# Kernel tuning notes

Measured on AMD Instinct MI355X. Metric: run time of the kernel, lower is better.

Reference implementation:

```python
import jax, jax.numpy as jnp
import numpy as np
import math

TIN = 4          # patch_size
NF = 128         # num_features
DM = 256         # d_model
NH = 8           # n_heads
HD = DM // NH    # head_dim = 32
FF = 1024        # ff_dim
NL = 4           # num_layers
MAXD = 64        # max_rel_dist -> L = 129


def _ln(x, g, b, eps):
    mu = jnp.mean(x, axis=-1, keepdims=True)
    var = jnp.mean(jnp.square(x - mu), axis=-1, keepdims=True)
    return (x - mu) * jax.lax.rsqrt(var + eps) * g + b


def setup_inputs() -> dict:
    key = jax.random.key(0)
    ks = jax.random.split(key, 24)
    s = 0.02
    d = {
        'x': jax.random.normal(ks[0], (2000, 16, NF), jnp.float32),
        'ln1_g': jnp.ones((TIN * NF,), jnp.float32),
        'ln1_b': jnp.zeros((TIN * NF,), jnp.float32),
        'proj_w': jax.random.normal(ks[1], (TIN * NF, DM), jnp.float32) * s,
        'proj_b': jnp.zeros((DM,), jnp.float32),
        'ln2_g': jnp.ones((DM,), jnp.float32),
        'ln2_b': jnp.zeros((DM,), jnp.float32),
        'rel_bias': jax.random.normal(ks[2], (NH, 2 * MAXD + 1), jnp.float32) * s,
        'ln_attn_g': jnp.ones((NL, DM), jnp.float32),
        'ln_attn_b': jnp.zeros((NL, DM), jnp.float32),
        'qkv_w': jax.random.normal(ks[3], (NL, DM, 3 * DM), jnp.float32) * s,
        'qkv_b': jnp.zeros((NL, 3 * DM), jnp.float32),
        'out_w': jax.random.normal(ks[4], (NL, DM, DM), jnp.float32) * s,
        'out_b': jnp.zeros((NL, DM), jnp.float32),
        'ln_ff_g': jnp.ones((NL, DM), jnp.float32),
        'ln_ff_b': jnp.zeros((NL, DM), jnp.float32),
        'ff1_w': jax.random.normal(ks[5], (NL, DM, FF), jnp.float32) * s,
        'ff1_b': jnp.zeros((NL, FF), jnp.float32),
        'ff2_w': jax.random.normal(ks[6], (NL, FF, DM), jnp.float32) * s,
        'ff2_b': jnp.zeros((NL, DM), jnp.float32),
        'fln_g': jnp.ones((DM,), jnp.float32),
        'fln_b': jnp.zeros((DM,), jnp.float32),
        'op_w': jax.random.normal(ks[7], (DM, NF), jnp.float32) * s,
        'op_b': jnp.zeros((NF,), jnp.float32),
    }
    return d


def reference(x, ln1_g, ln1_b, proj_w, proj_b, ln2_g, ln2_b, rel_bias,
              ln_attn_g, ln_attn_b, qkv_w, qkv_b, out_w, out_b,
              ln_ff_g, ln_ff_b, ff1_w, ff1_b, ff2_w, ff2_b,
              fln_g, fln_b, op_w, op_b):
    # ---- PatchEmbedding ----
    h = jnp.swapaxes(x, 0, 1)                 # [B, T, F]
    B, T, F = h.shape
    n_patch = T // TIN                        # 500 (== chunk_size, single chunk path)
    h = h[:, :n_patch * TIN, :].reshape(B, n_patch, TIN * F)
    h = _ln(h, ln1_g, ln1_b, 1e-6)
    h = h @ proj_w + proj_b
    h = _ln(h, ln2_g, ln2_b, 1e-6)            # [B, S, DM]
    S = n_patch

    # ---- relative position bias [H, S, S] ----
    pos = jnp.arange(S)
    rel = pos[None, :] - pos[:, None]
    idx = jnp.clip(rel, -MAXD, MAXD) + MAXD
    bias = rel_bias[:, idx]                   # [H, S, S]

    # ---- causal mask ----
    causal = jnp.triu(jnp.full((S, S), -jnp.inf, jnp.float32), k=1)
    scale = 1.0 / math.sqrt(HD)

    for l in range(NL):
        # attention block
        a = _ln(h, ln_attn_g[l], ln_attn_b[l], 1e-5)
        qkv = a @ qkv_w[l] + qkv_b[l]         # [B, S, 3*DM]
        q, k, v = jnp.split(qkv, 3, axis=-1)
        q = q.reshape(B, S, NH, HD)
        k = k.reshape(B, S, NH, HD)
        v = v.reshape(B, S, NH, HD)
        scores = jnp.einsum('bihd,bjhd->bhij', q, k) * scale
        scores = scores + bias[None] + causal
        attn = jax.nn.softmax(scores, axis=-1)
        o = jnp.einsum('bhij,bjhd->bihd', attn, v).reshape(B, S, DM)
        h = h + (o @ out_w[l] + out_b[l])
        # ffn block
        f = _ln(h, ln_ff_g[l], ln_ff_b[l], 1e-5)
        f = jax.nn.gelu(f @ ff1_w[l] + ff1_b[l], approximate=False)
        h = h + (f @ ff2_w[l] + ff2_b[l])

    h = _ln(h, fln_g, fln_b, 1e-5)
    h = h @ op_w + op_b                       # [B, S, NF]
    return jnp.swapaxes(h, 0, 1)              # [S, B, NF]
```

## Files before the change

### kernel.cpp

```cpp
#include <hip/hip_runtime.h>

#define TS 500
#define NB 16
#define NROW 8000
#define DMODEL 256
#define NHEAD 8
#define HDIM 32
#define FFD 1024

typedef __bf16 bf16x8 __attribute__((ext_vector_type(8)));
typedef __bf16 bf16x4 __attribute__((ext_vector_type(4)));
typedef float  f32x4  __attribute__((ext_vector_type(4)));
typedef float  f32x2  __attribute__((ext_vector_type(2)));

__device__ __forceinline__ float wred_sum(float v) {
    #pragma unroll
    for (int off = 32; off; off >>= 1) v += __shfl_xor(v, off, 64);
    return v;
}

__device__ __forceinline__ void pa_store(__bf16* __restrict__ PA, int KS,
                                         int grow, int col, float y) {
    int mt = grow >> 4, rl = grow & 15;
    size_t idx = ((size_t)(mt * KS + (col >> 5)) * 64 + ((col >> 3) & 3) * 16 + rl) * 8 + (col & 7);
    PA[idx] = (__bf16)y;
}

__global__ __launch_bounds__(256) void k_pack_all(
    const float* __restrict__ qkv_w, const float* __restrict__ out_w,
    const float* __restrict__ ff1_w, const float* __restrict__ ff2_w,
    const float* __restrict__ proj_w, const float* __restrict__ op_w,
    __bf16* __restrict__ PBq, __bf16* __restrict__ PBo,
    __bf16* __restrict__ PB1, __bf16* __restrict__ PB2,
    __bf16* __restrict__ PBp, __bf16* __restrict__ PBop)
{
    int bid = blockIdx.x;
    const float* W; __bf16* PB; int KS, NT, wLS, pLS, l, bx;
    if (bid < 384)       { W = qkv_w;  PB = PBq;  KS = 8;  NT = 48; wLS = 196608; pLS = 196608; l = bid / 96;          bx = bid % 96; }
    else if (bid < 512)  { W = out_w;  PB = PBo;  KS = 8;  NT = 16; wLS = 65536;  pLS = 65536;  l = (bid - 384) / 32;  bx = (bid - 384) % 32; }
    else if (bid < 1024) { W = ff1_w;  PB = PB1;  KS = 8;  NT = 64; wLS = 262144; pLS = 262144; l = (bid - 512) / 128; bx = (bid - 512) % 128; }
    else if (bid < 1536) { W = ff2_w;  PB = PB2;  KS = 32; NT = 16; wLS = 262144; pLS = 262144; l = (bid - 1024) / 128; bx = (bid - 1024) % 128; }
    else if (bid < 1600) { W = proj_w; PB = PBp;  KS = 16; NT = 16; wLS = 0;      pLS = 0;      l = 0;                 bx = bid - 1536; }
    else                 { W = op_w;   PB = PBop; KS = 8;  NT = 8;  wLS = 0;      pLS = 0;      l = 0;                 bx = bid - 1600; }

    int gid = bx * 256 + threadIdx.x;
    if (gid >= NT * KS * 64) return;
    int lane = gid & 63;
    int ks = (gid >> 6) % KS;
    int nt = (gid >> 6) / KS;
    int N = NT * 16;
    int k0 = ks * 32 + (lane >> 4) * 8;
    int col = nt * 16 + (lane & 15);
    const float* src = W + (size_t)l * wLS;
    bf16x8 v;
    #pragma unroll
    for (int j = 0; j < 8; j++) v[j] = (__bf16)src[(size_t)(k0 + j) * N + col];
    *(bf16x8*)(PB + (size_t)l * pLS + ((size_t)(nt * KS + ks) * 64 + lane) * 8) = v;
}

__global__ __launch_bounds__(256) void k_patchfused(
    const float* __restrict__ x, const float* __restrict__ g1, const float* __restrict__ b1,
    const __bf16* __restrict__ PBp, const float* __restrict__ bias,
    float* __restrict__ h, __bf16* __restrict__ PAout,
    const float* __restrict__ gam, const float* __restrict__ bet,
    const float* __restrict__ gam2, const float* __restrict__ bet2)
{
    __shared__ __align__(16) __bf16 As[2][16][64][8];
    __shared__ float redS[4][32];
    __shared__ float redQ[4][32];
    int t = threadIdx.x, lane = t & 63, w = t >> 6;
    int row0 = blockIdx.x * 32;

    for (int rr = 0; rr < 8; rr++) {
        int lrow = w * 8 + rr;
        int row = row0 + lrow;
        int b = row / TS, p = row - b * TS;
        int kb = lane * 8;
        const float* src = x + ((size_t)(p * 4 + (kb >> 7)) * NB + b) * 128 + (kb & 127);
        float4 lo = *(const float4*)src;
        float4 hi = *(const float4*)(src + 4);
        float v[8] = {lo.x, lo.y, lo.z, lo.w, hi.x, hi.y, hi.z, hi.w};
        float s = 0.f;
        #pragma unroll
        for (int j = 0; j < 8; j++) s += v[j];
        s = wred_sum(s);
        float mu = s * (1.0f / 512.0f);
        float q = 0.f;
        #pragma unroll
        for (int j = 0; j < 8; j++) { float d = v[j] - mu; q += d * d; }
        q = wred_sum(q);
        float rs = rsqrtf(q * (1.0f / 512.0f) + 1e-6f);
        float4 gl = *(const float4*)(g1 + kb), gh = *(const float4*)(g1 + kb + 4);
        float4 bl = *(const float4*)(b1 + kb), bh = *(const float4*)(b1 + kb + 4);
        float gg[8] = {gl.x, gl.y, gl.z, gl.w, gh.x, gh.y, gh.z, gh.w};
        float bbv[8] = {bl.x, bl.y, bl.z, bl.w, bh.x, bh.y, bh.z, bh.w};
        bf16x8 yv;
        #pragma unroll
        for (int j = 0; j < 8; j++) yv[j] = (__bf16)((v[j] - mu) * rs * gg[j] + bbv[j]);
        *(bf16x8*)&As[lrow >> 4][lane >> 2][(lane & 3) * 16 + (lrow & 15)][0] = yv;
    }
    __syncthreads();

    const bf16x8* B8 = (const bf16x8*)PBp;
    f32x4 acc[2][4] = {};
    #pragma unroll 8
    for (int ks = 0; ks < 16; ks++) {
        bf16x8 a0 = *(const bf16x8*)&As[0][ks][lane][0];
        bf16x8 a1 = *(const bf16x8*)&As[1][ks][lane][0];
        #pragma unroll
        for (int n = 0; n < 4; n++) {
            bf16x8 b = B8[((size_t)(w * 4 + n) * 16 + ks) * 64 + lane];
            acc[0][n] = __builtin_amdgcn_mfma_f32_16x16x32_bf16(a0, b, acc[0][n], 0, 0, 0);
            acc[1][n] = __builtin_amdgcn_mfma_f32_16x16x32_bf16(a1, b, acc[1][n], 0, 0, 0);
        }
    }

    int g_ = lane >> 4, cl = lane & 15;
    int rbase = g_ * 4;
    int mt0 = blockIdx.x * 2;
    float gamv[4], betv[4], gam2v[4], bet2v[4];
    #pragma unroll
    for (int n = 0; n < 4; n++) {
        int col = (w * 4 + n) * 16 + cl;
        float bv = bias[col];
        gamv[n] = gam[col]; betv[n] = bet[col];
        gam2v[n] = gam2[col]; bet2v[n] = bet2[col];
        #pragma unroll
        for (int m = 0; m < 2; m++)
            #pragma unroll
            for (int r = 0; r < 4; r++) acc[m][n][r] += bv;
    }
    float mu[2][4], rstd[2][4];
    {
        float ps[2][4];
        #pragma unroll
        for (int m = 0; m < 2; m++)
            #pragma unroll
            for (int r = 0; r < 4; r++) {
                float s = acc[m][0][r] + acc[m][1][r] + acc[m][2][r] + acc[m][3][r];
                #pragma unroll
                for (int off = 1; off < 16; off <<= 1) s += __shfl_xor(s, off, 64);
                ps[m][r] = s;
            }
        if (cl == 0)
            #pragma unroll
            for (int m = 0; m < 2; m++)
                #pragma unroll
                for (int r = 0; r < 4; r++) redS[w][m * 16 + rbase + r] = ps[m][r];
        __syncthreads();
        #pragma unroll
        for (int m = 0; m < 2; m++)
            #pragma unroll
            for (int r = 0; r < 4; r++) {
                int lr = m * 16 + rbase + r;
                mu[m][r] = (redS[0][lr] + redS[1][lr] + redS[2][lr] + redS[3][lr]) * (1.0f / 256.0f);
            }
        float pq[2][4];
        #pragma unroll
        for (int m = 0; m < 2; m++)
            #pragma unroll
            for (int r = 0; r < 4; r++) {
                float s = 0.f;
                #pragma unroll
                for (int n = 0; n < 4; n++) { float d = acc[m][n][r] - mu[m][r]; s += d * d; }
                #pragma unroll
                for (int off = 1; off < 16; off <<= 1) s += __shfl_xor(s, off, 64);
                pq[m][r] = s;
            }
        if (cl == 0)
            #pragma unroll
            for (int m = 0; m < 2; m++)
                #pragma unroll
                for (int r = 0; r < 4; r++) redQ[w][m * 16 + rbase + r] = pq[m][r];
        __syncthreads();
        #pragma unroll
        for (int m = 0; m < 2; m++)
            #pragma unroll
            for (int r = 0; r < 4; r++) {
                int lr = m * 16 + rbase + r;
                float var = (redQ[0][lr] + redQ[1][lr] + redQ[2][lr] + redQ[3][lr]) * (1.0f / 256.0f);
                rstd[m][r] = rsqrtf(var + 1e-6f);
            }
    }
    float ps2[2][4];
    #pragma unroll
    for (int m = 0; m < 2; m++) {
        int row = (mt0 + m) * 16 + rbase;
        #pragma unroll
        for (int r = 0; r < 4; r++) {
            float s = 0.f;
            #pragma unroll
            for (int n = 0; n < 4; n++) {
                int col = (w * 4 + n) * 16 + cl;
                float y1 = (acc[m][n][r] - mu[m][r]) * rstd[m][r] * gamv[n] + betv[n];
                h[(size_t)(row + r) * 256 + col] = y1;
                s += y1;
            }
            #pragma unroll
            for (int off = 1; off < 16; off <<= 1) s += __shfl_xor(s, off, 64);
            ps2[m][r] = s;
        }
    }
    if (cl == 0)
        #pragma unroll
        for (int m = 0; m < 2; m++)
            #pragma unroll
            for (int r = 0; r < 4; r++) redS[w][m * 16 + rbase + r] = ps2[m][r];
    __syncthreads();
    float mu2[2][4], rstd2[2][4];
    #pragma unroll
    for (int m = 0; m < 2; m++)
        #pragma unroll
        for (int r = 0; r < 4; r++) {
            int lr = m * 16 + rbase + r;
            mu2[m][r] = (redS[0][lr] + redS[1][lr] + redS[2][lr] + redS[3][lr]) * (1.0f / 256.0f);
        }
    float pq2[2][4];
    #pragma unroll
    for (int m = 0; m < 2; m++)
        #pragma unroll
        for (int r = 0; r < 4; r++) {
            float s = 0.f;
            #pragma unroll
            for (int n = 0; n < 4; n++) {
                float y1 = (acc[m][n][r] - mu[m][r]) * rstd[m][r] * gamv[n] + betv[n];
                float d = y1 - mu2[m][r];
                s += d * d;
            }
            #pragma unroll
            for (int off = 1; off < 16; off <<= 1) s += __shfl_xor(s, off, 64);
            pq2[m][r] = s;
        }
    if (cl == 0)
        #pragma unroll
        for (int m = 0; m < 2; m++)
            #pragma unroll
            for (int r = 0; r < 4; r++) redQ[w][m * 16 + rbase + r] = pq2[m][r];
    __syncthreads();
    #pragma unroll
    for (int m = 0; m < 2; m++)
        #pragma unroll
        for (int r = 0; r < 4; r++) {
            int lr = m * 16 + rbase + r;
            float var = (redQ[0][lr] + redQ[1][lr] + redQ[2][lr] + redQ[3][lr]) * (1.0f / 256.0f);
            rstd2[m][r] = rsqrtf(var + 1e-5f);
        }
    #pragma unroll
    for (int m = 0; m < 2; m++) {
        int row = (mt0 + m) * 16 + rbase;
        #pragma unroll
        for (int n = 0; n < 4; n++) {
            int col = (w * 4 + n) * 16 + cl;
            #pragma unroll
            for (int r = 0; r < 4; r++) {
                float y1 = (acc[m][n][r] - mu[m][r]) * rstd[m][r] * gamv[n] + betv[n];
                float y2 = (y1 - mu2[m][r]) * rstd2[m][r] * gam2v[n] + bet2v[n];
                pa_store(PAout, 8, row + r, col, y2);
            }
        }
    }
}

template<int KS, int MT, int NTW, int EPI>
__global__ __launch_bounds__(256) void k_gemm(
    const __bf16* __restrict__ PA, const __bf16* __restrict__ PB,
    const float* __restrict__ bias, float* __restrict__ dst,
    __bf16* __restrict__ dstb,
    const float* __restrict__ gam, const float* __restrict__ bet)
{
    int t = threadIdx.x, lane = t & 63, w = t >> 6;
    int mt0 = blockIdx.x * MT;
    int ntBase = blockIdx.y * (4 * NTW) + w * NTW;

    const bf16x8* A8 = (const bf16x8*)PA;
    const bf16x8* B8 = (const bf16x8*)PB;

    f32x4 acc[MT][NTW] = {};

    #pragma unroll 8
    for (int ks = 0; ks < KS; ks++) {
        bf16x8 a[MT], b[NTW];
        #pragma unroll
        for (int m = 0; m < MT; m++)
            a[m] = A8[((size_t)(mt0 + m) * KS + ks) * 64 + lane];
        #pragma unroll
        for (int n = 0; n < NTW; n++)
            b[n] = B8[((size_t)(ntBase + n) * KS + ks) * 64 + lane];
        #pragma unroll
        for (int m = 0; m < MT; m++)
            #pragma unroll
            for (int n = 0; n < NTW; n++)
                acc[m][n] = __builtin_amdgcn_mfma_f32_16x16x32_bf16(a[m], b[n], acc[m][n], 0, 0, 0);
    }

    int g_ = lane >> 4, cl = lane & 15;
    int rbase = g_ * 4;

    if constexpr (EPI == 4) {
        __shared__ float redS[4][MT * 16];
        __shared__ float redQ[4][MT * 16];
        float gamv[NTW], betv[NTW];
        #pragma unroll
        for (int n = 0; n < NTW; n++) {
            int col = (ntBase + n) * 16 + cl;
            float bv = bias[col];
            gamv[n] = gam[col]; betv[n] = bet[col];
            #pragma unroll
            for (int m = 0; m < MT; m++) {
                int row = (mt0 + m) * 16 + rbase;
                #pragma unroll
                for (int r = 0; r < 4; r++) {
                    float v = acc[m][n][r] + bv + dst[(size_t)(row + r) * 256 + col];
                    dst[(size_t)(row + r) * 256 + col] = v;
                    acc[m][n][r] = v;
                }
            }
        }
        float mu[MT][4], rstd[MT][4];
        {
            float ps[MT][4];
            #pragma unroll
            for (int m = 0; m < MT; m++)
                #pragma unroll
                for (int r = 0; r < 4; r++) {
                    float s = 0.f;
                    #pragma unroll
                    for (int n = 0; n < NTW; n++) s += acc[m][n][r];
                    #pragma unroll
                    for (int off = 1; off < 16; off <<= 1) s += __shfl_xor(s, off, 64);
                    ps[m][r] = s;
                }
            if (cl == 0)
                #pragma unroll
                for (int m = 0; m < MT; m++)
                    #pragma unroll
                    for (int r = 0; r < 4; r++) redS[w][m * 16 + rbase + r] = ps[m][r];
            __syncthreads();
            #pragma unroll
            for (int m = 0; m < MT; m++)
                #pragma unroll
                for (int r = 0; r < 4; r++) {
                    int lr = m * 16 + rbase + r;
                    mu[m][r] = (redS[0][lr] + redS[1][lr] + redS[2][lr] + redS[3][lr]) * (1.0f / 256.0f);
                }
            float pq[MT][4];
            #pragma unroll
            for (int m = 0; m < MT; m++)
                #pragma unroll
                for (int r = 0; r < 4; r++) {
                    float s = 0.f;
                    #pragma unroll
                    for (int n = 0; n < NTW; n++) { float d = acc[m][n][r] - mu[m][r]; s += d * d; }
                    #pragma unroll
                    for (int off = 1; off < 16; off <<= 1) s += __shfl_xor(s, off, 64);
                    pq[m][r] = s;
                }
            if (cl == 0)
                #pragma unroll
                for (int m = 0; m < MT; m++)
                    #pragma unroll
                    for (int r = 0; r < 4; r++) redQ[w][m * 16 + rbase + r] = pq[m][r];
            __syncthreads();
            #pragma unroll
            for (int m = 0; m < MT; m++)
                #pragma unroll
                for (int r = 0; r < 4; r++) {
                    int lr = m * 16 + rbase + r;
                    float var = (redQ[0][lr] + redQ[1][lr] + redQ[2][lr] + redQ[3][lr]) * (1.0f / 256.0f);
                    rstd[m][r] = rsqrtf(var + 1e-5f);
                }
        }
        #pragma unroll
        for (int m = 0; m < MT; m++) {
            int row = (mt0 + m) * 16 + rbase;
            #pragma unroll
            for (int n = 0; n < NTW; n++) {
                int col = (ntBase + n) * 16 + cl;
                #pragma unroll
                for (int r = 0; r < 4; r++) {
                    float y = (acc[m][n][r] - mu[m][r]) * rstd[m][r] * gamv[n] + betv[n];
                    pa_store(dstb, 8, row + r, col, y);
                }
            }
        }
    } else {
        #pragma unroll
        for (int m = 0; m < MT; m++) {
            int row = (mt0 + m) * 16 + rbase;
            #pragma unroll
            for (int n = 0; n < NTW; n++) {
                int col = (ntBase + n) * 16 + cl;
                float bv = bias[col];
                f32x4 v = acc[m][n];
                if (EPI == 0) {
                    #pragma unroll
                    for (int r = 0; r < 4; r++)
                        dstb[(size_t)(row + r) * 768 + col] = (__bf16)(v[r] + bv);
                } else {
                    #pragma unroll
                    for (int r = 0; r < 4; r++) {
                        int grow = row + r;
                        int bq = grow / TS, p = grow - bq * TS;
                        dst[((size_t)p * NB + bq) * 128 + col] = v[r] + bv;
                    }
                }
            }
        }
    }
}

__global__ __launch_bounds__(256) void k_fffused(
    const __bf16* __restrict__ PA, const __bf16* __restrict__ PB1,
    const float* __restrict__ b1, const __bf16* __restrict__ PB2,
    const float* __restrict__ b2, float* __restrict__ h,
    __bf16* __restrict__ PAout,
    const float* __restrict__ gam, const float* __restrict__ bet)
{
    __shared__ __align__(16) __bf16 F1s[2][32][64][8];
    __shared__ float redS[4][32];
    __shared__ float redQ[4][32];
    int t = threadIdx.x, lane = t & 63, w = t >> 6;
    int mt0 = blockIdx.x * 2;
    int g_ = lane >> 4, cl = lane & 15, rbase = g_ * 4;

    const bf16x8* A8 = (const bf16x8*)PA;
    const bf16x8* B81 = (const bf16x8*)PB1;
    const bf16x8* B82 = (const bf16x8*)PB2;

    f32x4 acc1[2][16] = {};
    for (int ks = 0; ks < 8; ks++) {
        bf16x8 a0 = A8[((size_t)mt0 * 8 + ks) * 64 + lane];
        bf16x8 a1 = A8[((size_t)(mt0 + 1) * 8 + ks) * 64 + lane];
        #pragma unroll
        for (int n = 0; n < 16; n++) {
            bf16x8 b = B81[((size_t)(w * 16 + n) * 8 + ks) * 64 + lane];
            acc1[0][n] = __builtin_amdgcn_mfma_f32_16x16x32_bf16(a0, b, acc1[0][n], 0, 0, 0);
            acc1[1][n] = __builtin_amdgcn_mfma_f32_16x16x32_bf16(a1, b, acc1[1][n], 0, 0, 0);
        }
    }
    #pragma unroll
    for (int n = 0; n < 16; n++) {
        int col = (w * 16 + n) * 16 + cl;
        float bv = b1[col];
        #pragma unroll
        for (int m = 0; m < 2; m++)
            #pragma unroll
            for (int r = 0; r < 4; r++) {
                float xx = acc1[m][n][r] + bv;
                float gl = 0.5f * xx * (1.0f + erff(xx * 0.70710678118654752f));
                F1s[m][col >> 5][((col >> 3) & 3) * 16 + rbase + r][col & 7] = (__bf16)gl;
            }
    }
    __syncthreads();

    f32x4 acc[2][4] = {};
    for (int ks = 0; ks < 32; ks++) {
        bf16x8 a0 = *(const bf16x8*)&F1s[0][ks][lane][0];
        bf16x8 a1 = *(const bf16x8*)&F1s[1][ks][lane][0];
        #pragma unroll
        for (int n = 0; n < 4; n++) {
            bf16x8 b = B82[((size_t)(w * 4 + n) * 32 + ks) * 64 + lane];
            acc[0][n] = __builtin_amdgcn_mfma_f32_16x16x32_bf16(a0, b, acc[0][n], 0, 0, 0);
            acc[1][n] = __builtin_amdgcn_mfma_f32_16x16x32_bf16(a1, b, acc[1][n], 0, 0, 0);
        }
    }

    float gamv[4], betv[4];
    #pragma unroll
    for (int n = 0; n < 4; n++) {
        int col = (w * 4 + n) * 16 + cl;
        float bv = b2[col];
        gamv[n] = gam[col]; betv[n] = bet[col];
        #pragma unroll
        for (int m = 0; m < 2; m++) {
            int row = (mt0 + m) * 16 + rbase;
            #pragma unroll
            for (int r = 0; r < 4; r++) {
                float v = acc[m][n][r] + bv + h[(size_t)(row + r) * 256 + col];
                h[(size_t)(row + r) * 256 + col] = v;
                acc[m][n][r] = v;
            }
        }
    }
    float mu[2][4], rstd[2][4];
    {
        float ps[2][4];
        #pragma unroll
        for (int m = 0; m < 2; m++)
            #pragma unroll
            for (int r = 0; r < 4; r++) {
                float s = acc[m][0][r] + acc[m][1][r] + acc[m][2][r] + acc[m][3][r];
                #pragma unroll
                for (int off = 1; off < 16; off <<= 1) s += __shfl_xor(s, off, 64);
                ps[m][r] = s;
            }
        if (cl == 0)
            #pragma unroll
            for (int m = 0; m < 2; m++)
                #pragma unroll
                for (int r = 0; r < 4; r++) redS[w][m * 16 + rbase + r] = ps[m][r];
        __syncthreads();
        #pragma unroll
        for (int m = 0; m < 2; m++)
            #pragma unroll
            for (int r = 0; r < 4; r++) {
                int lr = m * 16 + rbase + r;
                mu[m][r] = (redS[0][lr] + redS[1][lr] + redS[2][lr] + redS[3][lr]) * (1.0f / 256.0f);
            }
        float pq[2][4];
        #pragma unroll
        for (int m = 0; m < 2; m++)
            #pragma unroll
            for (int r = 0; r < 4; r++) {
                float s = 0.f;
                #pragma unroll
                for (int n = 0; n < 4; n++) { float d = acc[m][n][r] - mu[m][r]; s += d * d; }
                #pragma unroll
                for (int off = 1; off < 16; off <<= 1) s += __shfl_xor(s, off, 64);
                pq[m][r] = s;
            }
        if (cl == 0)
            #pragma unroll
            for (int m = 0; m < 2; m++)
                #pragma unroll
                for (int r = 0; r < 4; r++) redQ[w][m * 16 + rbase + r] = pq[m][r];
        __syncthreads();
        #pragma unroll
        for (int m = 0; m < 2; m++)
            #pragma unroll
            for (int r = 0; r < 4; r++) {
                int lr = m * 16 + rbase + r;
                float var = (redQ[0][lr] + redQ[1][lr] + redQ[2][lr] + redQ[3][lr]) * (1.0f / 256.0f);
                rstd[m][r] = rsqrtf(var + 1e-5f);
            }
    }
    #pragma unroll
    for (int m = 0; m < 2; m++) {
        int row = (mt0 + m) * 16 + rbase;
        #pragma unroll
        for (int n = 0; n < 4; n++) {
            int col = (w * 4 + n) * 16 + cl;
            #pragma unroll
            for (int r = 0; r < 4; r++) {
                float y = (acc[m][n][r] - mu[m][r]) * rstd[m][r] * gamv[n] + betv[n];
                pa_store(PAout, 8, row + r, col, y);
            }
        }
    }
}

__global__ __launch_bounds__(256) void k_attn(
    const __bf16* __restrict__ qkv, const float* __restrict__ rel_bias,
    __bf16* __restrict__ PA)
{
    __shared__ __align__(16) __bf16 Kfr[4][64][8];
    __shared__ __align__(16) __bf16 Vpl[2][64][16];
    __shared__ __align__(16) __bf16 PT[4][64][16];
    __shared__ float bias_s[132];

    int bh = blockIdx.x, qt = 7 - blockIdx.y;
    int b = bh >> 3, hh = bh & 7;
    int q0 = qt * 64;
    int t = threadIdx.x, lane = t & 63, w = t >> 6;
    int c = lane & 15, g = lane >> 4;

    const __bf16* base = qkv + (size_t)b * TS * 768 + hh * 32;

    if (t < 129) bias_s[t] = rel_bias[hh * 129 + t];

    bf16x8 aq = {};
    {
        int qi = q0 + 16 * w + c;
        if (qi < TS) aq = *(const bf16x8*)(base + (size_t)qi * 768 + 8 * g);
    }

    float lpart[4] = {0.f, 0.f, 0.f, 0.f};
    f32x4 O0 = {}, O1 = {};
    const float scale = 0.17677669529663687f;

    int nj = qt + 1;

    for (int it = 0; it < nj; it++) {
        int j0 = it * 64;
        __syncthreads();
        {
            int j = j0 + w * 16 + c;
            bf16x8 kv = {};
            if (j < TS) kv = *(const bf16x8*)(base + (size_t)j * 768 + 256 + 8 * g);
            *(bf16x8*)&Kfr[w][lane][0] = kv;
        }
        {
            int jl = t >> 2, dseg = t & 3;
            int j = j0 + jl;
            bf16x8 vv = {};
            if (j < TS) vv = *(const bf16x8*)(base + (size_t)j * 768 + 512 + 8 * dseg);
            *(bf16x8*)&Vpl[dseg >> 1][jl][(dseg & 1) * 8] = vv;
        }
        __syncthreads();

        f32x4 S[4];
        f32x4 zero = {};
        #pragma unroll
        for (int jt = 0; jt < 4; jt++) {
            bf16x8 bk = *(const bf16x8*)&Kfr[jt][lane][0];
            S[jt] = __builtin_amdgcn_mfma_f32_16x16x32_bf16(aq, bk, zero, 0, 0, 0);
        }

        #pragma unroll
        for (int jt = 0; jt < 4; jt++) {
            int j = j0 + jt * 16 + c;
            #pragma unroll
            for (int r = 0; r < 4; r++) {
                int i = q0 + 16 * w + 4 * g + r;
                int rel = j - i;
                rel = rel < -64 ? -64 : (rel > 64 ? 64 : rel);
                float sv = S[jt][r] * scale + bias_s[rel + 64];
                float p = (j > i) ? 0.f : __expf(sv);
                S[jt][r] = p;
                lpart[r] += p;
            }
        }

        #pragma unroll
        for (int jt = 0; jt < 4; jt++) {
            bf16x4 pv;
            pv[0] = (__bf16)S[jt][0]; pv[1] = (__bf16)S[jt][1];
            pv[2] = (__bf16)S[jt][2]; pv[3] = (__bf16)S[jt][3];
            *(bf16x4*)&PT[w][jt * 16 + c][4 * g] = pv;
        }
        asm volatile("s_waitcnt lgkmcnt(0)" ::: "memory");
        __builtin_amdgcn_sched_barrier(0);

        f32x2 pa_lo[2], pa_hi[2], vb_lo[2][2], vb_hi[2][2];
        #pragma unroll
        for (int jb = 0; jb < 2; jb++) {
            unsigned pta = (unsigned)(uintptr_t)&PT[w][jb * 32 + 8 * g][0] + c * 8;
            asm volatile("ds_read_b64_tr_b16 %0, %1" : "=v"(pa_lo[jb]) : "v"(pta) : "memory");
            asm volatile("ds_read_b64_tr_b16 %0, %1 offset:128" : "=v"(pa_hi[jb]) : "v"(pta) : "memory");
            #pragma unroll
            for (int dh = 0; dh < 2; dh++) {
                unsigned vta = (unsigned)(uintptr_t)&Vpl[dh][jb * 32 + 8 * g][0] + c * 8;
                asm volatile("ds_read_b64_tr_b16 %0, %1" : "=v"(vb_lo[jb][dh]) : "v"(vta) : "memory");
                asm volatile("ds_read_b64_tr_b16 %0, %1 offset:128" : "=v"(vb_hi[jb][dh]) : "v"(vta) : "memory");
            }
        }
        asm volatile("s_waitcnt lgkmcnt(0)" ::: "memory");
        __builtin_amdgcn_sched_barrier(0);

        #pragma unroll
        for (int jb = 0; jb < 2; jb++) {
            f32x4 pc = {pa_lo[jb][0], pa_lo[jb][1], pa_hi[jb][0], pa_hi[jb][1]};
            bf16x8 pa = __builtin_bit_cast(bf16x8, pc);
            f32x4 v0c = {vb_lo[jb][0][0], vb_lo[jb][0][1], vb_hi[jb][0][0], vb_hi[jb][0][1]};
            f32x4 v1c = {vb_lo[jb][1][0], vb_lo[jb][1][1], vb_hi[jb][1][0], vb_hi[jb][1][1]};
            bf16x8 vb0 = __builtin_bit_cast(bf16x8, v0c);
            bf16x8 vb1 = __builtin_bit_cast(bf16x8, v1c);
            O0 = __builtin_amdgcn_mfma_f32_16x16x32_bf16(pa, vb0, O0, 0, 0, 0);
            O1 = __builtin_amdgcn_mfma_f32_16x16x32_bf16(pa, vb1, O1, 0, 0, 0);
        }
    }

    #pragma unroll
    for (int r = 0; r < 4; r++) {
        #pragma unroll
        for (int off = 1; off < 16; off <<= 1) lpart[r] += __shfl_xor(lpart[r], off, 64);
    }
    #pragma unroll
    for (int r = 0; r < 4; r++) {
        int i = q0 + 16 * w + 4 * g + r;
        if (i < TS) {
            float inv = 1.0f / lpart[r];
            int grow = b * TS + i;
            int mt = grow >> 4, rl = grow & 15;
            size_t fb = (size_t)(mt * 8 + hh) * 64;
            PA[(fb + ((c >> 3) & 1) * 16 + rl) * 8 + (c & 7)]       = (__bf16)(O0[r] * inv);
            PA[(fb + (2 + ((c >> 3) & 1)) * 16 + rl) * 8 + (c & 7)] = (__bf16)(O1[r] * inv);
        }
    }
}

extern "C" void kernel_launch(void* const* d_in, const int* in_sizes, int n_in,
                              void* d_out, int out_size, void* d_ws, size_t ws_size,
                              hipStream_t stream)
{
    const float* x        = (const float*)d_in[0];
    const float* ln1_g    = (const float*)d_in[1];
    const float* ln1_b    = (const float*)d_in[2];
    const float* proj_w   = (const float*)d_in[3];
    const float* proj_b   = (const float*)d_in[4];
    const float* ln2_g    = (const float*)d_in[5];
    const float* ln2_b    = (const float*)d_in[6];
    const float* rel_bias = (const float*)d_in[7];
    const float* ln_attn_g= (const float*)d_in[8];
    const float* ln_attn_b= (const float*)d_in[9];
    const float* qkv_w    = (const float*)d_in[10];
    const float* qkv_b    = (const float*)d_in[11];
    const float* out_w    = (const float*)d_in[12];
    const float* out_b    = (const float*)d_in[13];
    const float* ln_ff_g  = (const float*)d_in[14];
    const float* ln_ff_b  = (const float*)d_in[15];
    const float* ff1_w    = (const float*)d_in[16];
    const float* ff1_b    = (const float*)d_in[17];
    const float* ff2_w    = (const float*)d_in[18];
    const float* ff2_b    = (const float*)d_in[19];
    const float* fln_g    = (const float*)d_in[20];
    const float* fln_b    = (const float*)d_in[21];
    const float* op_w     = (const float*)d_in[22];
    const float* op_b     = (const float*)d_in[23];
    float* out = (float*)d_out;

    char* ws = (char*)d_ws;
    float*  h     = (float*)(ws);
    __bf16* qkvb  = (__bf16*)(ws + 8192000);
    __bf16* PA    = (__bf16*)(ws + 20480000);
    __bf16* PBq   = (__bf16*)(ws + 24576000);
    __bf16* PBo   = (__bf16*)(ws + 26148864);
    __bf16* PB1   = (__bf16*)(ws + 26673152);
    __bf16* PB2   = (__bf16*)(ws + 28770304);
    __bf16* PBp   = (__bf16*)(ws + 30867456);
    __bf16* PBop  = (__bf16*)(ws + 31129600);

    k_pack_all<<<1616, 256, 0, stream>>>(qkv_w, out_w, ff1_w, ff2_w, proj_w, op_w,
                                         PBq, PBo, PB1, PB2, PBp, PBop);

    k_patchfused<<<250, 256, 0, stream>>>(x, ln1_g, ln1_b, PBp, proj_b, h, PA,
                                          ln2_g, ln2_b, ln_attn_g, ln_attn_b);

    for (int l = 0; l < 4; l++) {
        k_gemm<8, 2, 4, 0><<<dim3(250, 3), 256, 0, stream>>>(PA, PBq + (size_t)l * 196608,
                                                             qkv_b + l * 768, nullptr, qkvb,
                                                             nullptr, nullptr);
        dim3 ag(NB * NHEAD, 8);
        k_attn<<<ag, 256, 0, stream>>>(qkvb, rel_bias, PA);
        k_gemm<8, 2, 4, 4><<<dim3(250, 1), 256, 0, stream>>>(PA, PBo + (size_t)l * 65536,
                                                             out_b + l * 256, h, PA,
                                                             ln_ff_g + l * 256, ln_ff_b + l * 256);
        const float* ng = (l < 3) ? (ln_attn_g + (l + 1) * 256) : fln_g;
        const float* nb = (l < 3) ? (ln_attn_b + (l + 1) * 256) : fln_b;
        k_fffused<<<250, 256, 0, stream>>>(PA, PB1 + (size_t)l * 262144, ff1_b + l * 1024,
                                           PB2 + (size_t)l * 262144, ff2_b + l * 256,
                                           h, PA, ng, nb);
    }
    k_gemm<8, 2, 2, 5><<<dim3(250, 1), 256, 0, stream>>>(PA, PBop, op_b, out, nullptr,
                                                         nullptr, nullptr);
}
```

Measured before the change: 348.2 us.

## Halve rows per block in fused FFN and GEMMs, use LDS transpose reads

The fused FFN kernel now handles one 16-row tile per block instead of two, and the grid doubles to 500 blocks so more of the GPU's compute units are busy. The out-proj and output GEMMs also move to one M-tile per block on 500 blocks. The GELU intermediate is stored column-major in LDS with vector bf16x4 writes and read back with ds_read_b64_tr_b16 transpose loads, which avoids the scattered per-element packing stores. The cost is that each B-weight fragment is now reused by only one A-tile, so weight traffic per row doubles.

```diff
diff --git a/kernel.cpp b/kernel.cpp
--- a/kernel.cpp
+++ b/kernel.cpp
@@ -416,52 +416,62 @@
     __bf16* __restrict__ PAout,
     const float* __restrict__ gam, const float* __restrict__ bet)
 {
-    __shared__ __align__(16) __bf16 F1s[2][32][64][8];
-    __shared__ float redS[4][32];
-    __shared__ float redQ[4][32];
+    __shared__ __align__(16) __bf16 F1T[1024][16];
+    __shared__ float redS[4][16];
+    __shared__ float redQ[4][16];
     int t = threadIdx.x, lane = t & 63, w = t >> 6;
-    int mt0 = blockIdx.x * 2;
+    int mt = blockIdx.x;
     int g_ = lane >> 4, cl = lane & 15, rbase = g_ * 4;
 
     const bf16x8* A8 = (const bf16x8*)PA;
     const bf16x8* B81 = (const bf16x8*)PB1;
     const bf16x8* B82 = (const bf16x8*)PB2;
 
-    f32x4 acc1[2][16] = {};
+    f32x4 acc1[16] = {};
+    #pragma unroll 2
     for (int ks = 0; ks < 8; ks++) {
-        bf16x8 a0 = A8[((size_t)mt0 * 8 + ks) * 64 + lane];
-        bf16x8 a1 = A8[((size_t)(mt0 + 1) * 8 + ks) * 64 + lane];
+        bf16x8 a = A8[((size_t)mt * 8 + ks) * 64 + lane];
         #pragma unroll
         for (int n = 0; n < 16; n++) {
             bf16x8 b = B81[((size_t)(w * 16 + n) * 8 + ks) * 64 + lane];
-            acc1[0][n] = __builtin_amdgcn_mfma_f32_16x16x32_bf16(a0, b, acc1[0][n], 0, 0, 0);
-            acc1[1][n] = __builtin_amdgcn_mfma_f32_16x16x32_bf16(a1, b, acc1[1][n], 0, 0, 0);
+            acc1[n] = __builtin_amdgcn_mfma_f32_16x16x32_bf16(a, b, acc1[n], 0, 0, 0);
         }
     }
     #pragma unroll
     for (int n = 0; n < 16; n++) {
         int col = (w * 16 + n) * 16 + cl;
         float bv = b1[col];
-        #pragma unroll
-        for (int m = 0; m < 2; m++)
-            #pragma unroll
-            for (int r = 0; r < 4; r++) {
-                float xx = acc1[m][n][r] + bv;
-                float gl = 0.5f * xx * (1.0f + erff(xx * 0.70710678118654752f));
-                F1s[m][col >> 5][((col >> 3) & 3) * 16 + rbase + r][col & 7] = (__bf16)gl;
-            }
+        bf16x4 pv;
+        #pragma unroll
+        for (int r = 0; r < 4; r++) {
+            float xx = acc1[n][r] + bv;
+            pv[r] = (__bf16)(0.5f * xx * (1.0f + erff(xx * 0.70710678118654752f)));
+        }
+        *(bf16x4*)&F1T[col][rbase] = pv;
     }
     __syncthreads();
 
-    f32x4 acc[2][4] = {};
-    for (int ks = 0; ks < 32; ks++) {
-        bf16x8 a0 = *(const bf16x8*)&F1s[0][ks][lane][0];
-        bf16x8 a1 = *(const bf16x8*)&F1s[1][ks][lane][0];
-        #pragma unroll
-        for (int n = 0; n < 4; n++) {
-            bf16x8 b = B82[((size_t)(w * 4 + n) * 32 + ks) * 64 + lane];
-            acc[0][n] = __builtin_amdgcn_mfma_f32_16x16x32_bf16(a0, b, acc[0][n], 0, 0, 0);
-            acc[1][n] = __builtin_amdgcn_mfma_f32_16x16x32_bf16(a1, b, acc[1][n], 0, 0, 0);
+    f32x4 acc[4] = {};
+    for (int kb = 0; kb < 8; kb++) {
+        f32x2 lo[4], hi[4];
+        #pragma unroll
+        for (int q = 0; q < 4; q++) {
+            unsigned ta = (unsigned)(uintptr_t)&F1T[(kb * 4 + q) * 32 + 8 * g_][0] + cl * 8;
+            asm volatile("ds_read_b64_tr_b16 %0, %1" : "=v"(lo[q]) : "v"(ta) : "memory");
+            asm volatile("ds_read_b64_tr_b16 %0, %1 offset:128" : "=v"(hi[q]) : "v"(ta) : "memory");
+        }
+        asm volatile("s_waitcnt lgkmcnt(0)" ::: "memory");
+        __builtin_amdgcn_sched_barrier(0);
+        #pragma unroll
+        for (int q = 0; q < 4; q++) {
+            int ks = kb * 4 + q;
+            f32x4 pc = {lo[q][0], lo[q][1], hi[q][0], hi[q][1]};
+            bf16x8 a = __builtin_bit_cast(bf16x8, pc);
+            #pragma unroll
+            for (int n = 0; n < 4; n++) {
+                bf16x8 b = B82[((size_t)(w * 4 + n) * 32 + ks) * 64 + lane];
+                acc[n] = __builtin_amdgcn_mfma_f32_16x16x32_bf16(a, b, acc[n], 0, 0, 0);
+            }
         }
     }
 
@@ -471,80 +481,62 @@
         int col = (w * 4 + n) * 16 + cl;
         float bv = b2[col];
         gamv[n] = gam[col]; betv[n] = bet[col];
-        #pragma unroll
-        for (int m = 0; m < 2; m++) {
-            int row = (mt0 + m) * 16 + rbase;
-            #pragma unroll
-            for (int r = 0; r < 4; r++) {
-                float v = acc[m][n][r] + bv + h[(size_t)(row + r) * 256 + col];
-                h[(size_t)(row + r) * 256 + col] = v;
-                acc[m][n][r] = v;
-            }
-        }
-    }
-    float mu[2][4], rstd[2][4];
+        int row = mt * 16 + rbase;
+        #pragma unroll
+        for (int r = 0; r < 4; r++) {
+            float v = acc[n][r] + bv + h[(size_t)(row + r) * 256 + col];
+            h[(size_t)(row + r) * 256 + col] = v;
+            acc[n][r] = v;
+        }
+    }
+    float mu[4], rstd[4];
     {
-        float ps[2][4];
-        #pragma unroll
-        for (int m = 0; m < 2; m++)
-            #pragma unroll
-            for (int r = 0; r < 4; r++) {
-                float s = acc[m][0][r] + acc[m][1][r] + acc[m][2][r] + acc[m][3][r];
-                #pragma unroll
-                for (int off = 1; off < 16; off <<= 1) s += __shfl_xor(s, off, 64);
-                ps[m][r] = s;
-            }
+        float ps[4];
+        #pragma unroll
+        for (int r = 0; r < 4; r++) {
+            float s = acc[0][r] + acc[1][r] + acc[2][r] + acc[3][r];
+            #pragma unroll
+            for (int off = 1; off < 16; off <<= 1) s += __shfl_xor(s, off, 64);
+            ps[r] = s;
+        }
         if (cl == 0)
             #pragma unroll
-            for (int m = 0; m < 2; m++)
-                #pragma unroll
-                for (int r = 0; r < 4; r++) redS[w][m * 16 + rbase + r] = ps[m][r];
+            for (int r = 0; r < 4; r++) redS[w][rbase + r] = ps[r];
         __syncthreads();
         #pragma unroll
-        for (int m = 0; m < 2; m++)
-            #pragma unroll
-            for (int r = 0; r < 4; r++) {
-                int lr = m * 16 + rbase + r;
-                mu[m][r] = (redS[0][lr] + redS[1][lr] + redS[2][lr] + redS[3][lr]) * (1.0f / 256.0f);
-            }
-        float pq[2][4];
-        #pragma unroll
-        for (int m = 0; m < 2; m++)
-            #pragma unroll
-            for (int r = 0; r < 4; r++) {
-                float s = 0.f;
-                #pragma unroll
-                for (int n = 0; n < 4; n++) { float d = acc[m][n][r] - mu[m][r]; s += d * d; }
-                #pragma unroll
-                for (int off = 1; off < 16; off <<= 1) s += __shfl_xor(s, off, 64);
-                pq[m][r] = s;
-            }
+        for (int r = 0; r < 4; r++) {
+            int lr = rbase + r;
+            mu[r] = (redS[0][lr] + redS[1][lr] + redS[2][lr] + redS[3][lr]) * (1.0f / 256.0f);
+        }
+        float pq[4];
+        #pragma unroll
+        for (int r = 0; r < 4; r++) {
+            float s = 0.f;
+            #pragma unroll
+            for (int n = 0; n < 4; n++) { float d = acc[n][r] - mu[r]; s += d * d; }
+            #pragma unroll
+            for (int off = 1; off < 16; off <<= 1) s += __shfl_xor(s, off, 64);
+            pq[r] = s;
+        }
         if (cl == 0)
             #pragma unroll
-            for (int m = 0; m < 2; m++)
-                #pragma unroll
-                for (int r = 0; r < 4; r++) redQ[w][m * 16 + rbase + r] = pq[m][r];
+            for (int r = 0; r < 4; r++) redQ[w][rbase + r] = pq[r];
         __syncthreads();
         #pragma unroll
-        for (int m = 0; m < 2; m++)
-            #pragma unroll
-            for (int r = 0; r < 4; r++) {
-                int lr = m * 16 + rbase + r;
-                float var = (redQ[0][lr] + redQ[1][lr] + redQ[2][lr] + redQ[3][lr]) * (1.0f / 256.0f);
-                rstd[m][r] = rsqrtf(var + 1e-5f);
-            }
-    }
-    #pragma unroll
-    for (int m = 0; m < 2; m++) {
-        int row = (mt0 + m) * 16 + rbase;
-        #pragma unroll
-        for (int n = 0; n < 4; n++) {
-            int col = (w * 4 + n) * 16 + cl;
-            #pragma unroll
-            for (int r = 0; r < 4; r++) {
-                float y = (acc[m][n][r] - mu[m][r]) * rstd[m][r] * gamv[n] + betv[n];
-                pa_store(PAout, 8, row + r, col, y);
-            }
+        for (int r = 0; r < 4; r++) {
+            int lr = rbase + r;
+            float var = (redQ[0][lr] + redQ[1][lr] + redQ[2][lr] + redQ[3][lr]) * (1.0f / 256.0f);
+            rstd[r] = rsqrtf(var + 1e-5f);
+        }
+    }
+    int row = mt * 16 + rbase;
+    #pragma unroll
+    for (int n = 0; n < 4; n++) {
+        int col = (w * 4 + n) * 16 + cl;
+        #pragma unroll
+        for (int r = 0; r < 4; r++) {
+            float y = (acc[n][r] - mu[r]) * rstd[r] * gamv[n] + betv[n];
+            pa_store(PAout, 8, row + r, col, y);
         }
     }
 }
@@ -732,15 +724,15 @@
                                                              nullptr, nullptr);
         dim3 ag(NB * NHEAD, 8);
         k_attn<<<ag, 256, 0, stream>>>(qkvb, rel_bias, PA);
-        k_gemm<8, 2, 4, 4><<<dim3(250, 1), 256, 0, stream>>>(PA, PBo + (size_t)l * 65536,
+        k_gemm<8, 1, 4, 4><<<dim3(500, 1), 256, 0, stream>>>(PA, PBo + (size_t)l * 65536,
                                                              out_b + l * 256, h, PA,
                                                              ln_ff_g + l * 256, ln_ff_b + l * 256);
         const float* ng = (l < 3) ? (ln_attn_g + (l + 1) * 256) : fln_g;
         const float* nb = (l < 3) ? (ln_attn_b + (l + 1) * 256) : fln_b;
-        k_fffused<<<250, 256, 0, stream>>>(PA, PB1 + (size_t)l * 262144, ff1_b + l * 1024,
+        k_fffused<<<500, 256, 0, stream>>>(PA, PB1 + (size_t)l * 262144, ff1_b + l * 1024,
                                            PB2 + (size_t)l * 262144, ff2_b + l * 256,
                                            h, PA, ng, nb);
     }
-    k_gemm<8, 2, 2, 5><<<dim3(250, 1), 256, 0, stream>>>(PA, PBop, op_b, out, nullptr,
+    k_gemm<8, 1, 2, 5><<<dim3(500, 1), 256, 0, stream>>>(PA, PBop, op_b, out, nullptr,
                                                          nullptr, nullptr);
 }
```

After: 354.5 us. About the same (+1.8%).
